# Optimization experiments

Measured on AMD Instinct MI355X. Metric: run time of the kernel, lower is better.

Reference implementation:

```python
import jax, jax.numpy as jnp
import numpy as np

BS, SLEN = 4, 4096
H, ZD, VD = 8, 128, 256
CHUNK = 1024
NEG = -1e9


def _rope(x, cos, sin):
    # x: [B, S, H, D]; cos/sin: [S, D//2] (llama-style complex pair rotation)
    b, s, h, d = x.shape
    xr, xi = x.reshape(b, s, h, d // 2, 2)[..., 0], x.reshape(b, s, h, d // 2, 2)[..., 1]
    c = cos[None, :, None, :]
    sn = sin[None, :, None, :]
    orr = xr * c - xi * sn
    oii = xr * sn + xi * c
    return jnp.stack([orr, oii], axis=-1).reshape(b, s, h, d)


def setup_inputs() -> dict:
    key = jax.random.key(0)
    k1, k2, k3 = jax.random.split(key, 3)
    xq = jax.random.normal(k1, (BS, SLEN, H * ZD), dtype=jnp.float32)
    xk = jax.random.normal(k2, (BS, SLEN, H * ZD), dtype=jnp.float32)
    xv = jax.random.normal(k3, (BS, SLEN, H * VD), dtype=jnp.float32)
    # rotary tables over one chunk
    freqs = 1.0 / (10000.0 ** (np.arange(0, ZD, 2, dtype=np.float32) / ZD))  # [ZD//2]
    t = np.arange(CHUNK, dtype=np.float32)
    ang = np.outer(t, freqs)  # [CHUNK, ZD//2]
    cos = jnp.asarray(np.cos(ang), dtype=jnp.float32)
    sin = jnp.asarray(np.sin(ang), dtype=jnp.float32)
    # additive causal mask within a chunk
    causal = np.tril(np.ones((CHUNK, CHUNK), dtype=bool))
    mask = jnp.asarray(np.where(causal, 0.0, NEG).astype(np.float32))
    return {"xq": xq, "xk": xk, "xv": xv, "mask": mask, "cos": cos, "sin": sin}


def reference(xq, xk, xv, mask, cos, sin):
    bs, slen, _ = xq.shape
    nc = slen // CHUNK
    q = xq.reshape(bs * nc, CHUNK, H, ZD)
    k = xk.reshape(bs * nc, CHUNK, H, ZD)
    v = xv.reshape(bs * nc, CHUNK, H, VD)
    # RoPE applied after chunking (slen > chunk_size path)
    q = _rope(q, cos, sin)
    k = _rope(k, cos, sin)
    # block-local causal attention, no 1/sqrt(d) scaling (faithful to source)
    scores = jnp.einsum("bqhd,bkhd->bhqk", q, k) + mask[None, None, :, :]
    probs = jax.nn.softmax(scores.astype(jnp.float32), axis=-1).astype(q.dtype)
    out = jnp.einsum("bhqk,bkhd->bqhd", probs, v)
    return out.reshape(bs, slen, H * VD)
```

## Files before the change

### kernel.cpp

```cpp
#include <hip/hip_runtime.h>


#define NHEAD 8
#define ZDIM  128
#define VDIM  256
#define CHUNK 1024
#define QTILE 128
#define KT    32
#define NW    4

typedef _Float16 f16x8 __attribute__((ext_vector_type(8)));
typedef _Float16 f16x4 __attribute__((ext_vector_type(4)));
typedef __fp16   h16x2 __attribute__((ext_vector_type(2)));
typedef float    f32x4  __attribute__((ext_vector_type(4)));
typedef float    f32x16 __attribute__((ext_vector_type(16)));
typedef unsigned int u32;

#define KSTRIDE 128
#define VSTRIDE 36
#define LOG2E   1.44269504088896f
#define RTHR    11.5415603f

__global__ __launch_bounds__(256, 2)
void attn_fused(const float* __restrict__ xq, const float* __restrict__ xk,
                const float* __restrict__ xv, const float* __restrict__ cosT,
                const float* __restrict__ sinT, float* __restrict__ out)
{
  __shared__ _Float16 Klds[2][KT * KSTRIDE];
  __shared__ _Float16 Vlds[2][VDIM * VSTRIDE];

  const int b = (int)blockIdx.x;
  const int d = (b & 7) * 64 + (b >> 3);
  const int qpair = d & 3;
  const int ch = d >> 2;
  const int h  = ch & 7;
  const int cb = ch >> 3;

  const int tid  = threadIdx.x;
  const int w    = tid >> 6;
  const int lane = tid & 63;
  const int l31  = lane & 31;
  const int hi   = lane >> 5;
  const int vswz = (l31 >> 3) & 3;
  const int kswz = l31 & 7;

  const size_t row0 = (size_t)cb * CHUNK;

  const int kr    = tid >> 3;
  const int kt8   = tid & 7;
  const int vg    = tid >> 5;
  const int vc0   = (tid & 31) * 8;
  const int vsw   = tid & 3;
  const int vflip = ((tid >> 2) & 1) * 4;
  const int kblk  = vg >> 1;
  const int inb   = (vg & 1) * 4;

  int buf = 0;

  for (int half = 0; half < 2; ++half) {
    const int qt = half ? qpair : (7 - qpair);
    const int wq0 = qt * QTILE + w * 32;
    const int qg  = wq0 + l31;

    f16x8 qfrag[8];
    {
      const float* qp = xq + (row0 + qg) * (size_t)(NHEAD * ZDIM) + h * ZDIM;
      const float* cq = cosT + qg * (ZDIM / 2);
      const float* sq = sinT + qg * (ZDIM / 2);
#pragma unroll
      for (int dblk = 0; dblk < 8; ++dblk) {
        const int d0 = dblk * 16 + hi * 8;
        f32x4 a  = *(const f32x4*)(qp + d0);
        f32x4 b2 = *(const f32x4*)(qp + d0 + 4);
        f32x4 cv = *(const f32x4*)(cq + (d0 >> 1));
        f32x4 sv = *(const f32x4*)(sq + (d0 >> 1));
        union { h16x2 h2[4]; f16x8 v; } fr;
#pragma unroll
        for (int p = 0; p < 4; ++p) {
          const float xr = (p < 2 ? a[2 * p] : b2[2 * p - 4]);
          const float xi = (p < 2 ? a[2 * p + 1] : b2[2 * p - 3]);
          fr.h2[p] = __builtin_amdgcn_cvt_pkrtz((xr * cv[p] - xi * sv[p]) * LOG2E,
                                                (xr * sv[p] + xi * cv[p]) * LOG2E);
        }
        qfrag[dblk] = fr.v;
      }
    }

    const f32x16 zf = {};
    f32x16 acc[8];
#pragma unroll
    for (int g = 0; g < 8; ++g) acc[g] = zf;
    float mrun = -1e30f;
    float lrun = 0.f;

    const int nkt = 4 * (qt + 1);

    for (int kt = 0; kt < nkt; ++kt) {
      const int ktb = kt * KT;
      {
        const int krow = ktb + kr;
        const float* kpb = xk + (row0 + krow) * (size_t)(NHEAD * ZDIM) + h * ZDIM;
        const float* ckb = cosT + krow * (ZDIM / 2);
        const float* skb = sinT + krow * (ZDIM / 2);
        f32x4 a0 = *(const f32x4*)(kpb + 8 * kt8);
        f32x4 a1 = *(const f32x4*)(kpb + 8 * kt8 + 4);
        f32x4 ca = *(const f32x4*)(ckb + 4 * kt8);
        f32x4 sa = *(const f32x4*)(skb + 4 * kt8);
        f32x4 b0 = *(const f32x4*)(kpb + 8 * kt8 + 64);
        f32x4 b1 = *(const f32x4*)(kpb + 8 * kt8 + 68);
        f32x4 cbv = *(const f32x4*)(ckb + 4 * kt8 + 32);
        f32x4 sbv = *(const f32x4*)(skb + 4 * kt8 + 32);
        union { h16x2 h2[4]; f16x8 v; } koA, koB;
#pragma unroll
        for (int p = 0; p < 4; ++p) {
          const float xrA = (p < 2 ? a0[2 * p] : a1[2 * p - 4]);
          const float xiA = (p < 2 ? a0[2 * p + 1] : a1[2 * p - 3]);
          koA.h2[p] = __builtin_amdgcn_cvt_pkrtz(xrA * ca[p] - xiA * sa[p],
                                                 xrA * sa[p] + xiA * ca[p]);
          const float xrB = (p < 2 ? b0[2 * p] : b1[2 * p - 4]);
          const float xiB = (p < 2 ? b0[2 * p + 1] : b1[2 * p - 3]);
          koB.h2[p] = __builtin_amdgcn_cvt_pkrtz(xrB * cbv[p] - xiB * sbv[p],
                                                 xrB * sbv[p] + xiB * cbv[p]);
        }
        const int sw = kr & 7;
        *(f16x8*)&Klds[buf][kr * KSTRIDE + ((kt8 ^ sw) * 8)]       = koA.v;
        *(f16x8*)&Klds[buf][kr * KSTRIDE + (((kt8 + 8) ^ sw) * 8)] = koB.v;
      }
      {
        const int vrow = ktb + vg * 4;
        const float* vp = xv + (row0 + vrow) * (size_t)(NHEAD * VDIM) + h * VDIM + vc0;
        f32x4 v0 = *(const f32x4*)(vp);         f32x4 v1 = *(const f32x4*)(vp + 4);
        f32x4 v2 = *(const f32x4*)(vp + 2048);  f32x4 v3 = *(const f32x4*)(vp + 2052);
        f32x4 v4 = *(const f32x4*)(vp + 4096);  f32x4 v5 = *(const f32x4*)(vp + 4100);
        f32x4 v6 = *(const f32x4*)(vp + 6144);  f32x4 v7 = *(const f32x4*)(vp + 6148);
#pragma unroll
        for (int ci = 0; ci < 8; ++ci) {
          const float e0 = (ci < 4 ? v0[ci] : v1[ci - 4]);
          const float e1 = (ci < 4 ? v2[ci] : v3[ci - 4]);
          const float e2 = (ci < 4 ? v4[ci] : v5[ci - 4]);
          const float e3 = (ci < 4 ? v6[ci] : v7[ci - 4]);
          union { h16x2 a2[2]; f16x4 v; } t;
          t.a2[0] = __builtin_amdgcn_cvt_pkrtz(e0, e1);
          t.a2[1] = __builtin_amdgcn_cvt_pkrtz(e2, e3);
          *(f16x4*)&Vlds[buf][(vc0 + ci) * VSTRIDE + ((kblk ^ vsw) * 8) + (inb ^ vflip)] = t.v;
        }
      }
      __syncthreads();

      if (ktb <= wq0 + 31) {
        f32x16 s = {};
        __builtin_amdgcn_s_setprio(1);
#pragma unroll
        for (int dblk = 0; dblk < 8; ++dblk) {
          f16x8 kf = *(const f16x8*)&Klds[buf][l31 * KSTRIDE + (((dblk * 2 + hi) ^ kswz) * 8)];
          s = __builtin_amdgcn_mfma_f32_32x32x16_f16(kf, qfrag[dblk], s, 0, 0, 0);
        }
        __builtin_amdgcn_s_setprio(0);

        if (ktb + 31 > wq0) {
#pragma unroll
          for (int r = 0; r < 16; ++r) {
            const int kg = ktb + ((r & 3) + 8 * (r >> 2) + 4 * hi);
            if (kg > qg) s[r] = -1.0e9f;
          }
        }

        float m = s[0];
#pragma unroll
        for (int r = 1; r < 16; ++r) m = fmaxf(m, s[r]);
        m = fmaxf(m, __shfl_xor(m, 32));
        const bool need = (m > mrun + RTHR);
        if (__any(need)) {
          const float Mn = fmaxf(mrun, m);
          const float al = exp2f(mrun - Mn);
          mrun = Mn;
          lrun *= al;
#pragma unroll
          for (int r = 0; r < 16; ++r) {
            const float alr = __shfl(al, (r & 3) + 8 * (r >> 2) + 4 * hi);
#pragma unroll
            for (int g = 0; g < 8; ++g) acc[g][r] *= alr;
          }
        }
        float pr[16];
        float lsum = 0.f;
#pragma unroll
        for (int r = 0; r < 16; ++r) {
          pr[r] = exp2f(s[r] - mrun);
          lsum += pr[r];
        }
        lrun += lsum;

#pragma unroll
        for (int kb = 0; kb < 2; ++kb) {
          union { h16x2 h; u32 u; } A_, B_, C_, D_;
          A_.h = __builtin_amdgcn_cvt_pkrtz(pr[8 * kb + 0], pr[8 * kb + 1]);
          B_.h = __builtin_amdgcn_cvt_pkrtz(pr[8 * kb + 2], pr[8 * kb + 3]);
          C_.h = __builtin_amdgcn_cvt_pkrtz(pr[8 * kb + 4], pr[8 * kb + 5]);
          D_.h = __builtin_amdgcn_cvt_pkrtz(pr[8 * kb + 6], pr[8 * kb + 7]);
          const u32 G1 = hi ? A_.u : C_.u;
          const u32 G2 = hi ? B_.u : D_.u;
          const u32 G1s = (u32)__shfl_xor((int)G1, 32);
          const u32 G2s = (u32)__shfl_xor((int)G2, 32);
          union { u32 u[4]; f16x8 v; } af;
          af.u[0] = hi ? G1s : A_.u;
          af.u[1] = hi ? G2s : B_.u;
          af.u[2] = hi ? C_.u : G1s;
          af.u[3] = hi ? D_.u : G2s;
          __builtin_amdgcn_s_setprio(1);
#pragma unroll
          for (int g = 0; g < 8; ++g) {
            const int vcol = g * 32 + l31;
            const int ck = (((kb * 2 + hi) ^ vswz) * 8);
            const int fl = (g & 1) * 4;
            union { f16x4 h4[2]; f16x8 v; } bf;
            bf.h4[0] = *(const f16x4*)&Vlds[buf][vcol * VSTRIDE + ck + fl];
            bf.h4[1] = *(const f16x4*)&Vlds[buf][vcol * VSTRIDE + ck + (fl ^ 4)];
            acc[g] = __builtin_amdgcn_mfma_f32_32x32x16_f16(af.v, bf.v, acc[g], 0, 0, 0);
          }
          __builtin_amdgcn_s_setprio(0);
        }
      }
      buf ^= 1;
    }

    const float ls = lrun + __shfl_xor(lrun, 32);
    const float linv = 1.0f / ls;
#pragma unroll
    for (int r = 0; r < 16; ++r) {
      const int qloc = (r & 3) + 8 * (r >> 2) + 4 * hi;
      const float lr = __shfl(linv, qloc);
      const size_t ob = (row0 + wq0 + qloc) * (size_t)(NHEAD * VDIM) + h * VDIM + l31;
#pragma unroll
      for (int g = 0; g < 8; ++g)
        out[ob + g * 32] = acc[g][r] * lr;
    }
    __syncthreads();
  }
}

extern "C" void kernel_launch(void* const* d_in, const int* in_sizes, int n_in,
                              void* d_out, int out_size, void* d_ws, size_t ws_size,
                              hipStream_t stream) {
  const float* xq   = (const float*)d_in[0];
  const float* xk   = (const float*)d_in[1];
  const float* xv   = (const float*)d_in[2];
  const float* cosT = (const float*)d_in[4];
  const float* sinT = (const float*)d_in[5];
  float* out = (float*)d_out;

  dim3 grid(512);
  dim3 block(256);
  attn_fused<<<grid, block, 0, stream>>>(xq, xk, xv, cosT, sinT, out);
}
```

Measured before the change: 182.0 us.

## Split V columns across warps, shrink Q tile, drop paired-tile loop

Each block now handles a single 64-row query tile instead of a balanced pair of 128-row tiles, and each warp pair splits the 256-wide V output into two 128-column halves. This halves the per-warp accumulator registers, so occupancy can rise to three blocks per CU, and the grid grows to 2048 blocks scheduled heaviest-first. In exchange, the K/V loading and RoPE conversion are repeated by more blocks, and each warp pair recomputes the same QK^T scores and softmax.

```diff
diff --git a/kernel.cpp b/kernel.cpp
--- a/kernel.cpp
+++ b/kernel.cpp
@@ -5,7 +5,7 @@
 #define ZDIM  128
 #define VDIM  256
 #define CHUNK 1024
-#define QTILE 128
+#define QTILE 64
 #define KT    32
 #define NW    4
 
@@ -21,7 +21,7 @@
 #define LOG2E   1.44269504088896f
 #define RTHR    11.5415603f
 
-__global__ __launch_bounds__(256, 2)
+__global__ __launch_bounds__(256, 3)
 void attn_fused(const float* __restrict__ xq, const float* __restrict__ xk,
                 const float* __restrict__ xv, const float* __restrict__ cosT,
                 const float* __restrict__ sinT, float* __restrict__ out)
@@ -29,15 +29,17 @@
   __shared__ _Float16 Klds[2][KT * KSTRIDE];
   __shared__ _Float16 Vlds[2][VDIM * VSTRIDE];
 
-  const int b = (int)blockIdx.x;
-  const int d = (b & 7) * 64 + (b >> 3);
-  const int qpair = d & 3;
-  const int ch = d >> 2;
-  const int h  = ch & 7;
-  const int cb = ch >> 3;
+  const int b   = (int)blockIdx.x;
+  const int idx = b >> 3;
+  const int qt  = 15 - (idx >> 4);
+  const int ch  = (b & 7) * 16 + (idx & 15);
+  const int h   = ch & 7;
+  const int cb  = ch >> 3;
 
   const int tid  = threadIdx.x;
   const int w    = tid >> 6;
+  const int qg   = w >> 1;
+  const int vh   = w & 1;
   const int lane = tid & 63;
   const int l31  = lane & 31;
   const int hi   = lane >> 5;
@@ -55,187 +57,181 @@
   const int kblk  = vg >> 1;
   const int inb   = (vg & 1) * 4;
 
+  const int wq0 = qt * QTILE + qg * 32;
+  const int qgr = wq0 + l31;
+
+  f16x8 qfrag[8];
+  {
+    const float* qp = xq + (row0 + qgr) * (size_t)(NHEAD * ZDIM) + h * ZDIM;
+    const float* cq = cosT + qgr * (ZDIM / 2);
+    const float* sq = sinT + qgr * (ZDIM / 2);
+#pragma unroll
+    for (int dblk = 0; dblk < 8; ++dblk) {
+      const int d0 = dblk * 16 + hi * 8;
+      f32x4 a  = *(const f32x4*)(qp + d0);
+      f32x4 b2 = *(const f32x4*)(qp + d0 + 4);
+      f32x4 cv = *(const f32x4*)(cq + (d0 >> 1));
+      f32x4 sv = *(const f32x4*)(sq + (d0 >> 1));
+      union { h16x2 h2[4]; f16x8 v; } fr;
+#pragma unroll
+      for (int p = 0; p < 4; ++p) {
+        const float xr = (p < 2 ? a[2 * p] : b2[2 * p - 4]);
+        const float xi = (p < 2 ? a[2 * p + 1] : b2[2 * p - 3]);
+        fr.h2[p] = __builtin_amdgcn_cvt_pkrtz((xr * cv[p] - xi * sv[p]) * LOG2E,
+                                              (xr * sv[p] + xi * cv[p]) * LOG2E);
+      }
+      qfrag[dblk] = fr.v;
+    }
+  }
+
+  const f32x16 zf = {};
+  f32x16 acc[4];
+#pragma unroll
+  for (int g = 0; g < 4; ++g) acc[g] = zf;
+  float mrun = -1e30f;
+  float lrun = 0.f;
+
+  const int nkt = 2 * qt + 2;
   int buf = 0;
 
-  for (int half = 0; half < 2; ++half) {
-    const int qt = half ? qpair : (7 - qpair);
-    const int wq0 = qt * QTILE + w * 32;
-    const int qg  = wq0 + l31;
-
-    f16x8 qfrag[8];
+  for (int kt = 0; kt < nkt; ++kt) {
+    const int ktb = kt * KT;
     {
-      const float* qp = xq + (row0 + qg) * (size_t)(NHEAD * ZDIM) + h * ZDIM;
-      const float* cq = cosT + qg * (ZDIM / 2);
-      const float* sq = sinT + qg * (ZDIM / 2);
+      const int krow = ktb + kr;
+      const float* kpb = xk + (row0 + krow) * (size_t)(NHEAD * ZDIM) + h * ZDIM;
+      const float* ckb = cosT + krow * (ZDIM / 2);
+      const float* skb = sinT + krow * (ZDIM / 2);
+      f32x4 a0 = *(const f32x4*)(kpb + 8 * kt8);
+      f32x4 a1 = *(const f32x4*)(kpb + 8 * kt8 + 4);
+      f32x4 ca = *(const f32x4*)(ckb + 4 * kt8);
+      f32x4 sa = *(const f32x4*)(skb + 4 * kt8);
+      f32x4 b0 = *(const f32x4*)(kpb + 8 * kt8 + 64);
+      f32x4 b1 = *(const f32x4*)(kpb + 8 * kt8 + 68);
+      f32x4 cbv = *(const f32x4*)(ckb + 4 * kt8 + 32);
+      f32x4 sbv = *(const f32x4*)(skb + 4 * kt8 + 32);
+      union { h16x2 h2[4]; f16x8 v; } koA, koB;
+#pragma unroll
+      for (int p = 0; p < 4; ++p) {
+        const float xrA = (p < 2 ? a0[2 * p] : a1[2 * p - 4]);
+        const float xiA = (p < 2 ? a0[2 * p + 1] : a1[2 * p - 3]);
+        koA.h2[p] = __builtin_amdgcn_cvt_pkrtz(xrA * ca[p] - xiA * sa[p],
+                                               xrA * sa[p] + xiA * ca[p]);
+        const float xrB = (p < 2 ? b0[2 * p] : b1[2 * p - 4]);
+        const float xiB = (p < 2 ? b0[2 * p + 1] : b1[2 * p - 3]);
+        koB.h2[p] = __builtin_amdgcn_cvt_pkrtz(xrB * cbv[p] - xiB * sbv[p],
+                                               xrB * sbv[p] + xiB * cbv[p]);
+      }
+      const int sw = kr & 7;
+      *(f16x8*)&Klds[buf][kr * KSTRIDE + ((kt8 ^ sw) * 8)]       = koA.v;
+      *(f16x8*)&Klds[buf][kr * KSTRIDE + (((kt8 + 8) ^ sw) * 8)] = koB.v;
+    }
+    {
+      const int vrow = ktb + vg * 4;
+      const float* vp = xv + (row0 + vrow) * (size_t)(NHEAD * VDIM) + h * VDIM + vc0;
+      f32x4 v0 = *(const f32x4*)(vp);         f32x4 v1 = *(const f32x4*)(vp + 4);
+      f32x4 v2 = *(const f32x4*)(vp + 2048);  f32x4 v3 = *(const f32x4*)(vp + 2052);
+      f32x4 v4 = *(const f32x4*)(vp + 4096);  f32x4 v5 = *(const f32x4*)(vp + 4100);
+      f32x4 v6 = *(const f32x4*)(vp + 6144);  f32x4 v7 = *(const f32x4*)(vp + 6148);
+#pragma unroll
+      for (int ci = 0; ci < 8; ++ci) {
+        const float e0 = (ci < 4 ? v0[ci] : v1[ci - 4]);
+        const float e1 = (ci < 4 ? v2[ci] : v3[ci - 4]);
+        const float e2 = (ci < 4 ? v4[ci] : v5[ci - 4]);
+        const float e3 = (ci < 4 ? v6[ci] : v7[ci - 4]);
+        union { h16x2 a2[2]; f16x4 v; } t;
+        t.a2[0] = __builtin_amdgcn_cvt_pkrtz(e0, e1);
+        t.a2[1] = __builtin_amdgcn_cvt_pkrtz(e2, e3);
+        *(f16x4*)&Vlds[buf][(vc0 + ci) * VSTRIDE + ((kblk ^ vsw) * 8) + (inb ^ vflip)] = t.v;
+      }
+    }
+    __syncthreads();
+
+    if (ktb <= wq0 + 31) {
+      f32x16 s = {};
+      __builtin_amdgcn_s_setprio(1);
 #pragma unroll
       for (int dblk = 0; dblk < 8; ++dblk) {
-        const int d0 = dblk * 16 + hi * 8;
-        f32x4 a  = *(const f32x4*)(qp + d0);
-        f32x4 b2 = *(const f32x4*)(qp + d0 + 4);
-        f32x4 cv = *(const f32x4*)(cq + (d0 >> 1));
-        f32x4 sv = *(const f32x4*)(sq + (d0 >> 1));
-        union { h16x2 h2[4]; f16x8 v; } fr;
-#pragma unroll
-        for (int p = 0; p < 4; ++p) {
-          const float xr = (p < 2 ? a[2 * p] : b2[2 * p - 4]);
-          const float xi = (p < 2 ? a[2 * p + 1] : b2[2 * p - 3]);
-          fr.h2[p] = __builtin_amdgcn_cvt_pkrtz((xr * cv[p] - xi * sv[p]) * LOG2E,
-                                                (xr * sv[p] + xi * cv[p]) * LOG2E);
+        f16x8 kf = *(const f16x8*)&Klds[buf][l31 * KSTRIDE + (((dblk * 2 + hi) ^ kswz) * 8)];
+        s = __builtin_amdgcn_mfma_f32_32x32x16_f16(kf, qfrag[dblk], s, 0, 0, 0);
+      }
+      __builtin_amdgcn_s_setprio(0);
+
+      if (ktb + 31 > wq0) {
+#pragma unroll
+        for (int r = 0; r < 16; ++r) {
+          const int kg = ktb + ((r & 3) + 8 * (r >> 2) + 4 * hi);
+          if (kg > qgr) s[r] = -1.0e9f;
         }
-        qfrag[dblk] = fr.v;
-      }
-    }
-
-    const f32x16 zf = {};
-    f32x16 acc[8];
-#pragma unroll
-    for (int g = 0; g < 8; ++g) acc[g] = zf;
-    float mrun = -1e30f;
-    float lrun = 0.f;
-
-    const int nkt = 4 * (qt + 1);
-
-    for (int kt = 0; kt < nkt; ++kt) {
-      const int ktb = kt * KT;
-      {
-        const int krow = ktb + kr;
-        const float* kpb = xk + (row0 + krow) * (size_t)(NHEAD * ZDIM) + h * ZDIM;
-        const float* ckb = cosT + krow * (ZDIM / 2);
-        const float* skb = sinT + krow * (ZDIM / 2);
-        f32x4 a0 = *(const f32x4*)(kpb + 8 * kt8);
-        f32x4 a1 = *(const f32x4*)(kpb + 8 * kt8 + 4);
-        f32x4 ca = *(const f32x4*)(ckb + 4 * kt8);
-        f32x4 sa = *(const f32x4*)(skb + 4 * kt8);
-        f32x4 b0 = *(const f32x4*)(kpb + 8 * kt8 + 64);
-        f32x4 b1 = *(const f32x4*)(kpb + 8 * kt8 + 68);
-        f32x4 cbv = *(const f32x4*)(ckb + 4 * kt8 + 32);
-        f32x4 sbv = *(const f32x4*)(skb + 4 * kt8 + 32);
-        union { h16x2 h2[4]; f16x8 v; } koA, koB;
-#pragma unroll
-        for (int p = 0; p < 4; ++p) {
-          const float xrA = (p < 2 ? a0[2 * p] : a1[2 * p - 4]);
-          const float xiA = (p < 2 ? a0[2 * p + 1] : a1[2 * p - 3]);
-          koA.h2[p] = __builtin_amdgcn_cvt_pkrtz(xrA * ca[p] - xiA * sa[p],
-                                                 xrA * sa[p] + xiA * ca[p]);
-          const float xrB = (p < 2 ? b0[2 * p] : b1[2 * p - 4]);
-          const float xiB = (p < 2 ? b0[2 * p + 1] : b1[2 * p - 3]);
-          koB.h2[p] = __builtin_amdgcn_cvt_pkrtz(xrB * cbv[p] - xiB * sbv[p],
-                                                 xrB * sbv[p] + xiB * cbv[p]);
+      }
+
+      float m = s[0];
+#pragma unroll
+      for (int r = 1; r < 16; ++r) m = fmaxf(m, s[r]);
+      m = fmaxf(m, __shfl_xor(m, 32));
+      const bool need = (m > mrun + RTHR);
+      if (__any(need)) {
+        const float Mn = fmaxf(mrun, m);
+        const float al = exp2f(mrun - Mn);
+        mrun = Mn;
+        lrun *= al;
+#pragma unroll
+        for (int r = 0; r < 16; ++r) {
+          const float alr = __shfl(al, (r & 3) + 8 * (r >> 2) + 4 * hi);
+#pragma unroll
+          for (int g = 0; g < 4; ++g) acc[g][r] *= alr;
         }
-        const int sw = kr & 7;
-        *(f16x8*)&Klds[buf][kr * KSTRIDE + ((kt8 ^ sw) * 8)]       = koA.v;
-        *(f16x8*)&Klds[buf][kr * KSTRIDE + (((kt8 + 8) ^ sw) * 8)] = koB.v;
-      }
-      {
-        const int vrow = ktb + vg * 4;
-        const float* vp = xv + (row0 + vrow) * (size_t)(NHEAD * VDIM) + h * VDIM + vc0;
-        f32x4 v0 = *(const f32x4*)(vp);         f32x4 v1 = *(const f32x4*)(vp + 4);
-        f32x4 v2 = *(const f32x4*)(vp + 2048);  f32x4 v3 = *(const f32x4*)(vp + 2052);
-        f32x4 v4 = *(const f32x4*)(vp + 4096);  f32x4 v5 = *(const f32x4*)(vp + 4100);
-        f32x4 v6 = *(const f32x4*)(vp + 6144);  f32x4 v7 = *(const f32x4*)(vp + 6148);
-#pragma unroll
-        for (int ci = 0; ci < 8; ++ci) {
-          const float e0 = (ci < 4 ? v0[ci] : v1[ci - 4]);
-          const float e1 = (ci < 4 ? v2[ci] : v3[ci - 4]);
-          const float e2 = (ci < 4 ? v4[ci] : v5[ci - 4]);
-          const float e3 = (ci < 4 ? v6[ci] : v7[ci - 4]);
-          union { h16x2 a2[2]; f16x4 v; } t;
-          t.a2[0] = __builtin_amdgcn_cvt_pkrtz(e0, e1);
-          t.a2[1] = __builtin_amdgcn_cvt_pkrtz(e2, e3);
-          *(f16x4*)&Vlds[buf][(vc0 + ci) * VSTRIDE + ((kblk ^ vsw) * 8) + (inb ^ vflip)] = t.v;
-        }
-      }
-      __syncthreads();
-
-      if (ktb <= wq0 + 31) {
-        f32x16 s = {};
+      }
+      float lsum = 0.f;
+#pragma unroll
+      for (int r = 0; r < 16; ++r) {
+        s[r] = exp2f(s[r] - mrun);
+        lsum += s[r];
+      }
+      lrun += lsum;
+
+#pragma unroll
+      for (int kb = 0; kb < 2; ++kb) {
+        union { h16x2 h; u32 u; } A_, B_, C_, D_;
+        A_.h = __builtin_amdgcn_cvt_pkrtz(s[8 * kb + 0], s[8 * kb + 1]);
+        B_.h = __builtin_amdgcn_cvt_pkrtz(s[8 * kb + 2], s[8 * kb + 3]);
+        C_.h = __builtin_amdgcn_cvt_pkrtz(s[8 * kb + 4], s[8 * kb + 5]);
+        D_.h = __builtin_amdgcn_cvt_pkrtz(s[8 * kb + 6], s[8 * kb + 7]);
+        const u32 G1 = hi ? A_.u : C_.u;
+        const u32 G2 = hi ? B_.u : D_.u;
+        const u32 G1s = (u32)__shfl_xor((int)G1, 32);
+        const u32 G2s = (u32)__shfl_xor((int)G2, 32);
+        union { u32 u[4]; f16x8 v; } af;
+        af.u[0] = hi ? G1s : A_.u;
+        af.u[1] = hi ? G2s : B_.u;
+        af.u[2] = hi ? C_.u : G1s;
+        af.u[3] = hi ? D_.u : G2s;
         __builtin_amdgcn_s_setprio(1);
 #pragma unroll
-        for (int dblk = 0; dblk < 8; ++dblk) {
-          f16x8 kf = *(const f16x8*)&Klds[buf][l31 * KSTRIDE + (((dblk * 2 + hi) ^ kswz) * 8)];
-          s = __builtin_amdgcn_mfma_f32_32x32x16_f16(kf, qfrag[dblk], s, 0, 0, 0);
+        for (int g = 0; g < 4; ++g) {
+          const int vcol = vh * 128 + g * 32 + l31;
+          const int ck = (((kb * 2 + hi) ^ vswz) * 8);
+          const int fl = (g & 1) * 4;
+          union { f16x4 h4[2]; f16x8 v; } bf;
+          bf.h4[0] = *(const f16x4*)&Vlds[buf][vcol * VSTRIDE + ck + fl];
+          bf.h4[1] = *(const f16x4*)&Vlds[buf][vcol * VSTRIDE + ck + (fl ^ 4)];
+          acc[g] = __builtin_amdgcn_mfma_f32_32x32x16_f16(af.v, bf.v, acc[g], 0, 0, 0);
         }
         __builtin_amdgcn_s_setprio(0);
-
-        if (ktb + 31 > wq0) {
-#pragma unroll
-          for (int r = 0; r < 16; ++r) {
-            const int kg = ktb + ((r & 3) + 8 * (r >> 2) + 4 * hi);
-            if (kg > qg) s[r] = -1.0e9f;
-          }
-        }
-
-        float m = s[0];
-#pragma unroll
-        for (int r = 1; r < 16; ++r) m = fmaxf(m, s[r]);
-        m = fmaxf(m, __shfl_xor(m, 32));
-        const bool need = (m > mrun + RTHR);
-        if (__any(need)) {
-          const float Mn = fmaxf(mrun, m);
-          const float al = exp2f(mrun - Mn);
-          mrun = Mn;
-          lrun *= al;
-#pragma unroll
-          for (int r = 0; r < 16; ++r) {
-            const float alr = __shfl(al, (r & 3) + 8 * (r >> 2) + 4 * hi);
-#pragma unroll
-            for (int g = 0; g < 8; ++g) acc[g][r] *= alr;
-          }
-        }
-        float pr[16];
-        float lsum = 0.f;
-#pragma unroll
-        for (int r = 0; r < 16; ++r) {
-          pr[r] = exp2f(s[r] - mrun);
-          lsum += pr[r];
-        }
-        lrun += lsum;
-
-#pragma unroll
-        for (int kb = 0; kb < 2; ++kb) {
-          union { h16x2 h; u32 u; } A_, B_, C_, D_;
-          A_.h = __builtin_amdgcn_cvt_pkrtz(pr[8 * kb + 0], pr[8 * kb + 1]);
-          B_.h = __builtin_amdgcn_cvt_pkrtz(pr[8 * kb + 2], pr[8 * kb + 3]);
-          C_.h = __builtin_amdgcn_cvt_pkrtz(pr[8 * kb + 4], pr[8 * kb + 5]);
-          D_.h = __builtin_amdgcn_cvt_pkrtz(pr[8 * kb + 6], pr[8 * kb + 7]);
-          const u32 G1 = hi ? A_.u : C_.u;
-          const u32 G2 = hi ? B_.u : D_.u;
-          const u32 G1s = (u32)__shfl_xor((int)G1, 32);
-          const u32 G2s = (u32)__shfl_xor((int)G2, 32);
-          union { u32 u[4]; f16x8 v; } af;
-          af.u[0] = hi ? G1s : A_.u;
-          af.u[1] = hi ? G2s : B_.u;
-          af.u[2] = hi ? C_.u : G1s;
-          af.u[3] = hi ? D_.u : G2s;
-          __builtin_amdgcn_s_setprio(1);
-#pragma unroll
-          for (int g = 0; g < 8; ++g) {
-            const int vcol = g * 32 + l31;
-            const int ck = (((kb * 2 + hi) ^ vswz) * 8);
-            const int fl = (g & 1) * 4;
-            union { f16x4 h4[2]; f16x8 v; } bf;
-            bf.h4[0] = *(const f16x4*)&Vlds[buf][vcol * VSTRIDE + ck + fl];
-            bf.h4[1] = *(const f16x4*)&Vlds[buf][vcol * VSTRIDE + ck + (fl ^ 4)];
-            acc[g] = __builtin_amdgcn_mfma_f32_32x32x16_f16(af.v, bf.v, acc[g], 0, 0, 0);
-          }
-          __builtin_amdgcn_s_setprio(0);
-        }
-      }
-      buf ^= 1;
-    }
-
-    const float ls = lrun + __shfl_xor(lrun, 32);
-    const float linv = 1.0f / ls;
-#pragma unroll
-    for (int r = 0; r < 16; ++r) {
-      const int qloc = (r & 3) + 8 * (r >> 2) + 4 * hi;
-      const float lr = __shfl(linv, qloc);
-      const size_t ob = (row0 + wq0 + qloc) * (size_t)(NHEAD * VDIM) + h * VDIM + l31;
-#pragma unroll
-      for (int g = 0; g < 8; ++g)
-        out[ob + g * 32] = acc[g][r] * lr;
-    }
-    __syncthreads();
+      }
+    }
+    buf ^= 1;
+  }
+
+  const float ls = lrun + __shfl_xor(lrun, 32);
+  const float linv = 1.0f / ls;
+#pragma unroll
+  for (int r = 0; r < 16; ++r) {
+    const int qloc = (r & 3) + 8 * (r >> 2) + 4 * hi;
+    const float lr = __shfl(linv, qloc);
+    const size_t ob = (row0 + wq0 + qloc) * (size_t)(NHEAD * VDIM) + h * VDIM + vh * 128 + l31;
+#pragma unroll
+    for (int g = 0; g < 4; ++g)
+      out[ob + g * 32] = acc[g][r] * lr;
   }
 }
 
@@ -249,7 +245,7 @@
   const float* sinT = (const float*)d_in[5];
   float* out = (float*)d_out;
 
-  dim3 grid(512);
+  dim3 grid(2048);
   dim3 block(256);
   attn_fused<<<grid, block, 0, stream>>>(xq, xk, xv, cosT, sinT, out);
 }
```

Result: slower. 219.5 us (+20.6%).

## Precompute RoPE'd fp16 K and transposed fp16 V, stream via direct-to-LDS loads

Applied to the files above, without the earlier changes.

Adds two pre-pass kernels. One applies RoPE to K and writes it as fp16, the other transposes V into fp16 in a workspace. A new attention kernel then stages these tiles with global_load_lds async copies and explicit vmcnt waits for double buffering. The goal is to stop each block from redoing K rotation, V conversion and transposition, and to halve the bytes read per K/V tile. The cost is extra launches plus a full write and reread of K/V workspace, and the new path only runs when the workspace is large enough.

```diff
diff --git a/kernel.cpp b/kernel.cpp
--- a/kernel.cpp
+++ b/kernel.cpp
@@ -15,11 +15,276 @@
 typedef float    f32x4  __attribute__((ext_vector_type(4)));
 typedef float    f32x16 __attribute__((ext_vector_type(16)));
 typedef unsigned int u32;
+typedef unsigned int u32x4 __attribute__((ext_vector_type(4)));
 
 #define KSTRIDE 128
 #define VSTRIDE 36
 #define LOG2E   1.44269504088896f
 #define RTHR    11.5415603f
+
+#define KP_BYTES (128ULL * 1024 * 128 * 2)
+#define VT_BYTES (128ULL * 256 * 1024 * 2)
+
+__global__ __launch_bounds__(256)
+void prek(const float* __restrict__ xk, const float* __restrict__ cosT,
+          const float* __restrict__ sinT, _Float16* __restrict__ Kp)
+{
+  const int gid = blockIdx.x * 256 + threadIdx.x;
+  const int d0  = (gid & 15) * 8;
+  const int hh  = (gid >> 4) & 7;
+  const int row = gid >> 7;
+  const int krow = row & 1023;
+  const float* src = xk + (size_t)row * 1024 + hh * 128 + d0;
+  f32x4 a  = *(const f32x4*)src;
+  f32x4 b2 = *(const f32x4*)(src + 4);
+  f32x4 cv = *(const f32x4*)(cosT + krow * 64 + (d0 >> 1));
+  f32x4 sv = *(const f32x4*)(sinT + krow * 64 + (d0 >> 1));
+  union { h16x2 h2[4]; u32x4 v; } o;
+#pragma unroll
+  for (int p = 0; p < 4; ++p) {
+    const float xr = (p < 2 ? a[2 * p] : b2[2 * p - 4]);
+    const float xi = (p < 2 ? a[2 * p + 1] : b2[2 * p - 3]);
+    o.h2[p] = __builtin_amdgcn_cvt_pkrtz(xr * cv[p] - xi * sv[p],
+                                         xr * sv[p] + xi * cv[p]);
+  }
+  const int ghead = (row >> 10) * 8 + hh;
+  *(u32x4*)&Kp[((size_t)ghead * 1024 + krow) * 128 + d0] = o.v;
+}
+
+__global__ __launch_bounds__(256)
+void prev(const float* __restrict__ xv, _Float16* __restrict__ Vt)
+{
+  __shared__ float T[64][68];
+  const int bid = blockIdx.x;
+  const int vt  = bid & 3;
+  const int ktile = (bid >> 2) & 15;
+  const int hh  = (bid >> 6) & 7;
+  const int cbb = bid >> 9;
+  const int t = threadIdx.x;
+  {
+    const int kr2 = t >> 2, cg = (t & 3) * 16;
+    const float* src = xv + ((size_t)(cbb * 1024 + ktile * 64 + kr2)) * 2048
+                          + hh * 256 + vt * 64 + cg;
+    f32x4 r0 = *(const f32x4*)(src);
+    f32x4 r1 = *(const f32x4*)(src + 4);
+    f32x4 r2 = *(const f32x4*)(src + 8);
+    f32x4 r3 = *(const f32x4*)(src + 12);
+    *(f32x4*)&T[kr2][cg]      = r0;
+    *(f32x4*)&T[kr2][cg + 4]  = r1;
+    *(f32x4*)&T[kr2][cg + 8]  = r2;
+    *(f32x4*)&T[kr2][cg + 12] = r3;
+  }
+  __syncthreads();
+  {
+    const int vc2 = t >> 2, kg = (t & 3) * 16;
+    union { h16x2 h2[8]; u32x4 v[2]; } o;
+#pragma unroll
+    for (int m = 0; m < 8; ++m)
+      o.h2[m] = __builtin_amdgcn_cvt_pkrtz(T[kg + 2 * m][vc2], T[kg + 2 * m + 1][vc2]);
+    _Float16* dst = Vt + ((size_t)((cbb * 8 + hh) * 256 + vt * 64 + vc2)) * 1024
+                       + ktile * 64 + kg;
+    *(u32x4*)(dst)     = o.v[0];
+    *(u32x4*)(dst + 8) = o.v[1];
+  }
+}
+
+__device__ __forceinline__ void gld16(const _Float16* g, _Float16* l) {
+  __builtin_amdgcn_global_load_lds(
+      (const __attribute__((address_space(1))) u32*)g,
+      (__attribute__((address_space(3))) u32*)l, 16, 0, 0);
+}
+
+__global__ __launch_bounds__(256, 2)
+void attn_pre(const float* __restrict__ xq, const _Float16* __restrict__ Kp,
+              const _Float16* __restrict__ Vt, const float* __restrict__ cosT,
+              const float* __restrict__ sinT, float* __restrict__ out)
+{
+  __shared__ _Float16 Klds[2][KT * 128];
+  __shared__ _Float16 Vlds[2][VDIM * 32];
+
+  const int b = (int)blockIdx.x;
+  const int d = (b & 7) * 64 + (b >> 3);
+  const int qpair = d & 3;
+  const int ch = d >> 2;
+  const int h  = ch & 7;
+  const int cb = ch >> 3;
+  const int ghead = cb * 8 + h;
+
+  const int tid  = threadIdx.x;
+  const int w    = tid >> 6;
+  const int lane = tid & 63;
+  const int l31  = lane & 31;
+  const int hi   = lane >> 5;
+  const int kswz = l31 & 7;
+
+  const size_t row0 = (size_t)cb * CHUNK;
+  const _Float16* Kph = Kp + (size_t)ghead * 1024 * 128;
+  const _Float16* Vth = Vt + (size_t)ghead * 256 * 1024;
+
+  const int kr0  = w * 4 + (lane >> 4);
+  const int slot = lane & 15;
+  const int kchk = ((slot & 7) ^ (kr0 & 7)) | (slot & 8);
+  const int koff = kr0 * 128 + kchk * 8;
+  const int vcol0 = w * 16 + (lane >> 2);
+  const int vs    = lane & 3;
+  const int kbs   = vs ^ ((vcol0 >> 1) & 3);
+  const int voff  = vcol0 * 1024 + kbs * 8;
+
+  int buf = 0;
+
+#define STAGE(bufi, ktb_)                                            \
+  do {                                                               \
+    const _Float16* kb_ = Kph + (size_t)(ktb_) * 128 + koff;         \
+    gld16(kb_,        &Klds[bufi][w * 512]);                         \
+    gld16(kb_ + 2048, &Klds[bufi][2048 + w * 512]);                  \
+    const _Float16* vb_ = Vth + (ktb_) + voff;                       \
+    gld16(vb_,           &Vlds[bufi][w * 512]);                      \
+    gld16(vb_ + 65536,   &Vlds[bufi][2048 + w * 512]);               \
+    gld16(vb_ + 131072,  &Vlds[bufi][4096 + w * 512]);               \
+    gld16(vb_ + 196608,  &Vlds[bufi][6144 + w * 512]);               \
+  } while (0)
+
+  for (int half = 0; half < 2; ++half) {
+    const int qt = half ? qpair : (7 - qpair);
+    const int wq0 = qt * QTILE + w * 32;
+    const int qgr = wq0 + l31;
+
+    buf = 0;
+    STAGE(0, 0);
+
+    f16x8 qfrag[8];
+    {
+      const float* qp = xq + (row0 + qgr) * (size_t)(NHEAD * ZDIM) + h * ZDIM;
+      const float* cq = cosT + qgr * (ZDIM / 2);
+      const float* sq = sinT + qgr * (ZDIM / 2);
+#pragma unroll
+      for (int dblk = 0; dblk < 8; ++dblk) {
+        const int d0 = dblk * 16 + hi * 8;
+        f32x4 a  = *(const f32x4*)(qp + d0);
+        f32x4 b2 = *(const f32x4*)(qp + d0 + 4);
+        f32x4 cv = *(const f32x4*)(cq + (d0 >> 1));
+        f32x4 sv = *(const f32x4*)(sq + (d0 >> 1));
+        union { h16x2 h2[4]; f16x8 v; } fr;
+#pragma unroll
+        for (int p = 0; p < 4; ++p) {
+          const float xr = (p < 2 ? a[2 * p] : b2[2 * p - 4]);
+          const float xi = (p < 2 ? a[2 * p + 1] : b2[2 * p - 3]);
+          fr.h2[p] = __builtin_amdgcn_cvt_pkrtz((xr * cv[p] - xi * sv[p]) * LOG2E,
+                                                (xr * sv[p] + xi * cv[p]) * LOG2E);
+        }
+        qfrag[dblk] = fr.v;
+      }
+    }
+
+    const f32x16 zf = {};
+    f32x16 acc[8];
+#pragma unroll
+    for (int g = 0; g < 8; ++g) acc[g] = zf;
+    float mrun = -1e30f;
+    float lrun = 0.f;
+
+    const int nkt = 4 * (qt + 1);
+
+    for (int kt = 0; kt < nkt; ++kt) {
+      const int ktb = kt * KT;
+      if (kt + 1 < nkt) {
+        STAGE(buf ^ 1, ktb + KT);
+        asm volatile("s_waitcnt vmcnt(6)" ::: "memory");
+      } else {
+        asm volatile("s_waitcnt vmcnt(0)" ::: "memory");
+      }
+      __builtin_amdgcn_sched_barrier(0);
+      __builtin_amdgcn_s_barrier();
+
+      if (ktb <= wq0 + 31) {
+        f32x16 s = {};
+        __builtin_amdgcn_s_setprio(1);
+#pragma unroll
+        for (int dblk = 0; dblk < 8; ++dblk) {
+          f16x8 kf = *(const f16x8*)&Klds[buf][l31 * 128 + (((dblk * 2 + hi) ^ kswz) * 8)];
+          s = __builtin_amdgcn_mfma_f32_32x32x16_f16(kf, qfrag[dblk], s, 0, 0, 0);
+        }
+        __builtin_amdgcn_s_setprio(0);
+
+        if (ktb + 31 > wq0) {
+#pragma unroll
+          for (int r = 0; r < 16; ++r) {
+            const int kg = ktb + ((r & 3) + 8 * (r >> 2) + 4 * hi);
+            if (kg > qgr) s[r] = -1.0e9f;
+          }
+        }
+
+        float m = s[0];
+#pragma unroll
+        for (int r = 1; r < 16; ++r) m = fmaxf(m, s[r]);
+        m = fmaxf(m, __shfl_xor(m, 32));
+        const bool need = (m > mrun + RTHR);
+        if (__any(need)) {
+          const float Mn = fmaxf(mrun, m);
+          const float al = exp2f(mrun - Mn);
+          mrun = Mn;
+          lrun *= al;
+#pragma unroll
+          for (int r = 0; r < 16; ++r) {
+            const float alr = __shfl(al, (r & 3) + 8 * (r >> 2) + 4 * hi);
+#pragma unroll
+            for (int g = 0; g < 8; ++g) acc[g][r] *= alr;
+          }
+        }
+        float lsum = 0.f;
+#pragma unroll
+        for (int r = 0; r < 16; ++r) {
+          s[r] = exp2f(s[r] - mrun);
+          lsum += s[r];
+        }
+        lrun += lsum;
+
+#pragma unroll
+        for (int kb = 0; kb < 2; ++kb) {
+          union { h16x2 h; u32 u; } A_, B_, C_, D_;
+          A_.h = __builtin_amdgcn_cvt_pkrtz(s[8 * kb + 0], s[8 * kb + 1]);
+          B_.h = __builtin_amdgcn_cvt_pkrtz(s[8 * kb + 2], s[8 * kb + 3]);
+          C_.h = __builtin_amdgcn_cvt_pkrtz(s[8 * kb + 4], s[8 * kb + 5]);
+          D_.h = __builtin_amdgcn_cvt_pkrtz(s[8 * kb + 6], s[8 * kb + 7]);
+          const u32 G1 = hi ? A_.u : C_.u;
+          const u32 G2 = hi ? B_.u : D_.u;
+          const u32 G1s = (u32)__shfl_xor((int)G1, 32);
+          const u32 G2s = (u32)__shfl_xor((int)G2, 32);
+          union { u32 u[4]; f16x8 v; } af;
+          af.u[0] = hi ? G1s : A_.u;
+          af.u[1] = hi ? G2s : B_.u;
+          af.u[2] = hi ? C_.u : G1s;
+          af.u[3] = hi ? D_.u : G2s;
+          __builtin_amdgcn_s_setprio(1);
+#pragma unroll
+          for (int g = 0; g < 8; ++g) {
+            const int vcol = g * 32 + l31;
+            const int srd = ((kb * 2 + hi) ^ ((vcol >> 1) & 3)) * 8;
+            f16x8 bf = *(const f16x8*)&Vlds[buf][vcol * 32 + srd];
+            acc[g] = __builtin_amdgcn_mfma_f32_32x32x16_f16(af.v, bf, acc[g], 0, 0, 0);
+          }
+          __builtin_amdgcn_s_setprio(0);
+        }
+      }
+      __builtin_amdgcn_s_barrier();
+      buf ^= 1;
+    }
+
+    const float ls = lrun + __shfl_xor(lrun, 32);
+    const float linv = 1.0f / ls;
+#pragma unroll
+    for (int r = 0; r < 16; ++r) {
+      const int qloc = (r & 3) + 8 * (r >> 2) + 4 * hi;
+      const float lr = __shfl(linv, qloc);
+      const size_t ob = (row0 + wq0 + qloc) * (size_t)(NHEAD * VDIM) + h * VDIM + l31;
+#pragma unroll
+      for (int g = 0; g < 8; ++g)
+        out[ob + g * 32] = acc[g][r] * lr;
+    }
+    __builtin_amdgcn_s_barrier();
+  }
+#undef STAGE
+}
 
 __global__ __launch_bounds__(256, 2)
 void attn_fused(const float* __restrict__ xq, const float* __restrict__ xk,
@@ -60,13 +325,13 @@
   for (int half = 0; half < 2; ++half) {
     const int qt = half ? qpair : (7 - qpair);
     const int wq0 = qt * QTILE + w * 32;
-    const int qg  = wq0 + l31;
+    const int qgr = wq0 + l31;
 
     f16x8 qfrag[8];
     {
-      const float* qp = xq + (row0 + qg) * (size_t)(NHEAD * ZDIM) + h * ZDIM;
-      const float* cq = cosT + qg * (ZDIM / 2);
-      const float* sq = sinT + qg * (ZDIM / 2);
+      const float* qp = xq + (row0 + qgr) * (size_t)(NHEAD * ZDIM) + h * ZDIM;
+      const float* cq = cosT + qgr * (ZDIM / 2);
+      const float* sq = sinT + qgr * (ZDIM / 2);
 #pragma unroll
       for (int dblk = 0; dblk < 8; ++dblk) {
         const int d0 = dblk * 16 + hi * 8;
@@ -161,7 +426,7 @@
 #pragma unroll
           for (int r = 0; r < 16; ++r) {
             const int kg = ktb + ((r & 3) + 8 * (r >> 2) + 4 * hi);
-            if (kg > qg) s[r] = -1.0e9f;
+            if (kg > qgr) s[r] = -1.0e9f;
           }
         }
 
@@ -182,22 +447,21 @@
             for (int g = 0; g < 8; ++g) acc[g][r] *= alr;
           }
         }
-        float pr[16];
         float lsum = 0.f;
 #pragma unroll
         for (int r = 0; r < 16; ++r) {
-          pr[r] = exp2f(s[r] - mrun);
-          lsum += pr[r];
+          s[r] = exp2f(s[r] - mrun);
+          lsum += s[r];
         }
         lrun += lsum;
 
 #pragma unroll
         for (int kb = 0; kb < 2; ++kb) {
           union { h16x2 h; u32 u; } A_, B_, C_, D_;
-          A_.h = __builtin_amdgcn_cvt_pkrtz(pr[8 * kb + 0], pr[8 * kb + 1]);
-          B_.h = __builtin_amdgcn_cvt_pkrtz(pr[8 * kb + 2], pr[8 * kb + 3]);
-          C_.h = __builtin_amdgcn_cvt_pkrtz(pr[8 * kb + 4], pr[8 * kb + 5]);
-          D_.h = __builtin_amdgcn_cvt_pkrtz(pr[8 * kb + 6], pr[8 * kb + 7]);
+          A_.h = __builtin_amdgcn_cvt_pkrtz(s[8 * kb + 0], s[8 * kb + 1]);
+          B_.h = __builtin_amdgcn_cvt_pkrtz(s[8 * kb + 2], s[8 * kb + 3]);
+          C_.h = __builtin_amdgcn_cvt_pkrtz(s[8 * kb + 4], s[8 * kb + 5]);
+          D_.h = __builtin_amdgcn_cvt_pkrtz(s[8 * kb + 6], s[8 * kb + 7]);
           const u32 G1 = hi ? A_.u : C_.u;
           const u32 G2 = hi ? B_.u : D_.u;
           const u32 G1s = (u32)__shfl_xor((int)G1, 32);
@@ -249,7 +513,13 @@
   const float* sinT = (const float*)d_in[5];
   float* out = (float*)d_out;
 
-  dim3 grid(512);
-  dim3 block(256);
-  attn_fused<<<grid, block, 0, stream>>>(xq, xk, xv, cosT, sinT, out);
+  if (ws_size >= (size_t)(KP_BYTES + VT_BYTES)) {
+    _Float16* Kp = (_Float16*)d_ws;
+    _Float16* Vt = (_Float16*)((char*)d_ws + KP_BYTES);
+    prek<<<dim3(8192), dim3(256), 0, stream>>>(xk, cosT, sinT, Kp);
+    prev<<<dim3(8192), dim3(256), 0, stream>>>(xv, Vt);
+    attn_pre<<<dim3(512), dim3(256), 0, stream>>>(xq, Kp, Vt, cosT, sinT, out);
+  } else {
+    attn_fused<<<dim3(512), dim3(256), 0, stream>>>(xq, xk, xv, cosT, sinT, out);
+  }
 }
```

Result: slower. 338.5 us (+86.0%).

## Use single-buffered 64-key tiles with two barriers instead of double-buffered 32-key tiles

Applied to the files above, without the earlier changes.

Replaces the double-buffered 32-row K/V LDS tiles with one 64-row tile per iteration, processed as two 32-row sub-steps. A barrier now sits at the top of each iteration as well as after staging. This halves the number of loop iterations and amortizes barrier and staging overhead over more MFMA work, and LDS usage stays about the same. In exchange, loads for the next tile can no longer overlap with compute on the current one, and the causal tail is coarser (some 32-row halves are staged but skipped).

```diff
diff --git a/kernel.cpp b/kernel.cpp
--- a/kernel.cpp
+++ b/kernel.cpp
@@ -6,7 +6,7 @@
 #define VDIM  256
 #define CHUNK 1024
 #define QTILE 128
-#define KT    32
+#define KT64  64
 #define NW    4
 
 typedef _Float16 f16x8 __attribute__((ext_vector_type(8)));
@@ -17,7 +17,7 @@
 typedef unsigned int u32;
 
 #define KSTRIDE 128
-#define VSTRIDE 36
+#define VSTRIDE 68
 #define LOG2E   1.44269504088896f
 #define RTHR    11.5415603f
 
@@ -26,8 +26,8 @@
                 const float* __restrict__ xv, const float* __restrict__ cosT,
                 const float* __restrict__ sinT, float* __restrict__ out)
 {
-  __shared__ _Float16 Klds[2][KT * KSTRIDE];
-  __shared__ _Float16 Vlds[2][VDIM * VSTRIDE];
+  __shared__ _Float16 Klds[KT64 * KSTRIDE];
+  __shared__ _Float16 Vlds[VDIM * VSTRIDE];
 
   const int b = (int)blockIdx.x;
   const int d = (b & 7) * 64 + (b >> 3);
@@ -52,21 +52,19 @@
   const int vc0   = (tid & 31) * 8;
   const int vsw   = tid & 3;
   const int vflip = ((tid >> 2) & 1) * 4;
-  const int kblk  = vg >> 1;
+  const int kblk2 = vg >> 1;
   const int inb   = (vg & 1) * 4;
-
-  int buf = 0;
 
   for (int half = 0; half < 2; ++half) {
     const int qt = half ? qpair : (7 - qpair);
     const int wq0 = qt * QTILE + w * 32;
-    const int qg  = wq0 + l31;
+    const int qgr = wq0 + l31;
 
     f16x8 qfrag[8];
     {
-      const float* qp = xq + (row0 + qg) * (size_t)(NHEAD * ZDIM) + h * ZDIM;
-      const float* cq = cosT + qg * (ZDIM / 2);
-      const float* sq = sinT + qg * (ZDIM / 2);
+      const float* qp = xq + (row0 + qgr) * (size_t)(NHEAD * ZDIM) + h * ZDIM;
+      const float* cq = cosT + qgr * (ZDIM / 2);
+      const float* sq = sinT + qgr * (ZDIM / 2);
 #pragma unroll
       for (int dblk = 0; dblk < 8; ++dblk) {
         const int d0 = dblk * 16 + hi * 8;
@@ -93,66 +91,77 @@
     float mrun = -1e30f;
     float lrun = 0.f;
 
-    const int nkt = 4 * (qt + 1);
-
-    for (int kt = 0; kt < nkt; ++kt) {
-      const int ktb = kt * KT;
-      {
-        const int krow = ktb + kr;
-        const float* kpb = xk + (row0 + krow) * (size_t)(NHEAD * ZDIM) + h * ZDIM;
-        const float* ckb = cosT + krow * (ZDIM / 2);
-        const float* skb = sinT + krow * (ZDIM / 2);
-        f32x4 a0 = *(const f32x4*)(kpb + 8 * kt8);
-        f32x4 a1 = *(const f32x4*)(kpb + 8 * kt8 + 4);
-        f32x4 ca = *(const f32x4*)(ckb + 4 * kt8);
-        f32x4 sa = *(const f32x4*)(skb + 4 * kt8);
-        f32x4 b0 = *(const f32x4*)(kpb + 8 * kt8 + 64);
-        f32x4 b1 = *(const f32x4*)(kpb + 8 * kt8 + 68);
-        f32x4 cbv = *(const f32x4*)(ckb + 4 * kt8 + 32);
-        f32x4 sbv = *(const f32x4*)(skb + 4 * kt8 + 32);
-        union { h16x2 h2[4]; f16x8 v; } koA, koB;
-#pragma unroll
-        for (int p = 0; p < 4; ++p) {
-          const float xrA = (p < 2 ? a0[2 * p] : a1[2 * p - 4]);
-          const float xiA = (p < 2 ? a0[2 * p + 1] : a1[2 * p - 3]);
-          koA.h2[p] = __builtin_amdgcn_cvt_pkrtz(xrA * ca[p] - xiA * sa[p],
-                                                 xrA * sa[p] + xiA * ca[p]);
-          const float xrB = (p < 2 ? b0[2 * p] : b1[2 * p - 4]);
-          const float xiB = (p < 2 ? b0[2 * p + 1] : b1[2 * p - 3]);
-          koB.h2[p] = __builtin_amdgcn_cvt_pkrtz(xrB * cbv[p] - xiB * sbv[p],
-                                                 xrB * sbv[p] + xiB * cbv[p]);
-        }
-        const int sw = kr & 7;
-        *(f16x8*)&Klds[buf][kr * KSTRIDE + ((kt8 ^ sw) * 8)]       = koA.v;
-        *(f16x8*)&Klds[buf][kr * KSTRIDE + (((kt8 + 8) ^ sw) * 8)] = koB.v;
-      }
-      {
-        const int vrow = ktb + vg * 4;
-        const float* vp = xv + (row0 + vrow) * (size_t)(NHEAD * VDIM) + h * VDIM + vc0;
-        f32x4 v0 = *(const f32x4*)(vp);         f32x4 v1 = *(const f32x4*)(vp + 4);
-        f32x4 v2 = *(const f32x4*)(vp + 2048);  f32x4 v3 = *(const f32x4*)(vp + 2052);
-        f32x4 v4 = *(const f32x4*)(vp + 4096);  f32x4 v5 = *(const f32x4*)(vp + 4100);
-        f32x4 v6 = *(const f32x4*)(vp + 6144);  f32x4 v7 = *(const f32x4*)(vp + 6148);
-#pragma unroll
-        for (int ci = 0; ci < 8; ++ci) {
-          const float e0 = (ci < 4 ? v0[ci] : v1[ci - 4]);
-          const float e1 = (ci < 4 ? v2[ci] : v3[ci - 4]);
-          const float e2 = (ci < 4 ? v4[ci] : v5[ci - 4]);
-          const float e3 = (ci < 4 ? v6[ci] : v7[ci - 4]);
-          union { h16x2 a2[2]; f16x4 v; } t;
-          t.a2[0] = __builtin_amdgcn_cvt_pkrtz(e0, e1);
-          t.a2[1] = __builtin_amdgcn_cvt_pkrtz(e2, e3);
-          *(f16x4*)&Vlds[buf][(vc0 + ci) * VSTRIDE + ((kblk ^ vsw) * 8) + (inb ^ vflip)] = t.v;
+    const int n64 = 2 * (qt + 1);
+
+    for (int kt = 0; kt < n64; ++kt) {
+      const int ktb64 = kt * KT64;
+      __syncthreads();
+
+#pragma unroll
+      for (int p2 = 0; p2 < 2; ++p2) {
+        const int krow = ktb64 + p2 * 32 + kr;
+        {
+          const float* kpb = xk + (row0 + krow) * (size_t)(NHEAD * ZDIM) + h * ZDIM;
+          const float* ckb = cosT + krow * (ZDIM / 2);
+          const float* skb = sinT + krow * (ZDIM / 2);
+          f32x4 a0 = *(const f32x4*)(kpb + 8 * kt8);
+          f32x4 a1 = *(const f32x4*)(kpb + 8 * kt8 + 4);
+          f32x4 ca = *(const f32x4*)(ckb + 4 * kt8);
+          f32x4 sa = *(const f32x4*)(skb + 4 * kt8);
+          f32x4 b0 = *(const f32x4*)(kpb + 8 * kt8 + 64);
+          f32x4 b1 = *(const f32x4*)(kpb + 8 * kt8 + 68);
+          f32x4 cbv = *(const f32x4*)(ckb + 4 * kt8 + 32);
+          f32x4 sbv = *(const f32x4*)(skb + 4 * kt8 + 32);
+          union { h16x2 h2[4]; f16x8 v; } koA, koB;
+#pragma unroll
+          for (int p = 0; p < 4; ++p) {
+            const float xrA = (p < 2 ? a0[2 * p] : a1[2 * p - 4]);
+            const float xiA = (p < 2 ? a0[2 * p + 1] : a1[2 * p - 3]);
+            koA.h2[p] = __builtin_amdgcn_cvt_pkrtz(xrA * ca[p] - xiA * sa[p],
+                                                   xrA * sa[p] + xiA * ca[p]);
+            const float xrB = (p < 2 ? b0[2 * p] : b1[2 * p - 4]);
+            const float xiB = (p < 2 ? b0[2 * p + 1] : b1[2 * p - 3]);
+            koB.h2[p] = __builtin_amdgcn_cvt_pkrtz(xrB * cbv[p] - xiB * sbv[p],
+                                                   xrB * sbv[p] + xiB * cbv[p]);
+          }
+          const int lrow = p2 * 32 + kr;
+          const int sw = lrow & 7;
+          *(f16x8*)&Klds[lrow * KSTRIDE + ((kt8 ^ sw) * 8)]       = koA.v;
+          *(f16x8*)&Klds[lrow * KSTRIDE + (((kt8 + 8) ^ sw) * 8)] = koB.v;
+        }
+        {
+          const int vrow = ktb64 + p2 * 32 + vg * 4;
+          const float* vp = xv + (row0 + vrow) * (size_t)(NHEAD * VDIM) + h * VDIM + vc0;
+          f32x4 v0 = *(const f32x4*)(vp);         f32x4 v1 = *(const f32x4*)(vp + 4);
+          f32x4 v2 = *(const f32x4*)(vp + 2048);  f32x4 v3 = *(const f32x4*)(vp + 2052);
+          f32x4 v4 = *(const f32x4*)(vp + 4096);  f32x4 v5 = *(const f32x4*)(vp + 4100);
+          f32x4 v6 = *(const f32x4*)(vp + 6144);  f32x4 v7 = *(const f32x4*)(vp + 6148);
+          const int slot = ((kblk2 ^ vsw) * 8) + p2 * 32;
+#pragma unroll
+          for (int ci = 0; ci < 8; ++ci) {
+            const float e0 = (ci < 4 ? v0[ci] : v1[ci - 4]);
+            const float e1 = (ci < 4 ? v2[ci] : v3[ci - 4]);
+            const float e2 = (ci < 4 ? v4[ci] : v5[ci - 4]);
+            const float e3 = (ci < 4 ? v6[ci] : v7[ci - 4]);
+            union { h16x2 a2[2]; f16x4 v; } t;
+            t.a2[0] = __builtin_amdgcn_cvt_pkrtz(e0, e1);
+            t.a2[1] = __builtin_amdgcn_cvt_pkrtz(e2, e3);
+            *(f16x4*)&Vlds[(vc0 + ci) * VSTRIDE + slot + (inb ^ vflip)] = t.v;
+          }
         }
       }
       __syncthreads();
 
-      if (ktb <= wq0 + 31) {
+#pragma unroll
+      for (int s2 = 0; s2 < 2; ++s2) {
+        const int ktb = ktb64 + s2 * 32;
+        if (ktb > wq0 + 31) continue;
+
         f32x16 s = {};
         __builtin_amdgcn_s_setprio(1);
 #pragma unroll
         for (int dblk = 0; dblk < 8; ++dblk) {
-          f16x8 kf = *(const f16x8*)&Klds[buf][l31 * KSTRIDE + (((dblk * 2 + hi) ^ kswz) * 8)];
+          f16x8 kf = *(const f16x8*)&Klds[(s2 * 32 + l31) * KSTRIDE + (((dblk * 2 + hi) ^ kswz) * 8)];
           s = __builtin_amdgcn_mfma_f32_32x32x16_f16(kf, qfrag[dblk], s, 0, 0, 0);
         }
         __builtin_amdgcn_s_setprio(0);
@@ -161,7 +170,7 @@
 #pragma unroll
           for (int r = 0; r < 16; ++r) {
             const int kg = ktb + ((r & 3) + 8 * (r >> 2) + 4 * hi);
-            if (kg > qg) s[r] = -1.0e9f;
+            if (kg > qgr) s[r] = -1.0e9f;
           }
         }
 
@@ -182,22 +191,21 @@
             for (int g = 0; g < 8; ++g) acc[g][r] *= alr;
           }
         }
-        float pr[16];
         float lsum = 0.f;
 #pragma unroll
         for (int r = 0; r < 16; ++r) {
-          pr[r] = exp2f(s[r] - mrun);
-          lsum += pr[r];
+          s[r] = exp2f(s[r] - mrun);
+          lsum += s[r];
         }
         lrun += lsum;
 
 #pragma unroll
         for (int kb = 0; kb < 2; ++kb) {
           union { h16x2 h; u32 u; } A_, B_, C_, D_;
-          A_.h = __builtin_amdgcn_cvt_pkrtz(pr[8 * kb + 0], pr[8 * kb + 1]);
-          B_.h = __builtin_amdgcn_cvt_pkrtz(pr[8 * kb + 2], pr[8 * kb + 3]);
-          C_.h = __builtin_amdgcn_cvt_pkrtz(pr[8 * kb + 4], pr[8 * kb + 5]);
-          D_.h = __builtin_amdgcn_cvt_pkrtz(pr[8 * kb + 6], pr[8 * kb + 7]);
+          A_.h = __builtin_amdgcn_cvt_pkrtz(s[8 * kb + 0], s[8 * kb + 1]);
+          B_.h = __builtin_amdgcn_cvt_pkrtz(s[8 * kb + 2], s[8 * kb + 3]);
+          C_.h = __builtin_amdgcn_cvt_pkrtz(s[8 * kb + 4], s[8 * kb + 5]);
+          D_.h = __builtin_amdgcn_cvt_pkrtz(s[8 * kb + 6], s[8 * kb + 7]);
           const u32 G1 = hi ? A_.u : C_.u;
           const u32 G2 = hi ? B_.u : D_.u;
           const u32 G1s = (u32)__shfl_xor((int)G1, 32);
@@ -211,17 +219,16 @@
 #pragma unroll
           for (int g = 0; g < 8; ++g) {
             const int vcol = g * 32 + l31;
-            const int ck = (((kb * 2 + hi) ^ vswz) * 8);
+            const int ck = (((kb * 2 + hi) ^ vswz) * 8) + s2 * 32;
             const int fl = (g & 1) * 4;
             union { f16x4 h4[2]; f16x8 v; } bf;
-            bf.h4[0] = *(const f16x4*)&Vlds[buf][vcol * VSTRIDE + ck + fl];
-            bf.h4[1] = *(const f16x4*)&Vlds[buf][vcol * VSTRIDE + ck + (fl ^ 4)];
+            bf.h4[0] = *(const f16x4*)&Vlds[vcol * VSTRIDE + ck + fl];
+            bf.h4[1] = *(const f16x4*)&Vlds[vcol * VSTRIDE + ck + (fl ^ 4)];
             acc[g] = __builtin_amdgcn_mfma_f32_32x32x16_f16(af.v, bf.v, acc[g], 0, 0, 0);
           }
           __builtin_amdgcn_s_setprio(0);
         }
       }
-      buf ^= 1;
     }
 
     const float ls = lrun + __shfl_xor(lrun, 32);
```

After: 195.6 us. +7.5%, slower.
